# Kernel tuning notes

Hardware: AMD Instinct MI355X
Metric: run time of the kernel (lower is better)

Reference implementation:

```python
import jax, jax.numpy as jnp
import numpy as np

HEAD_SIZE = 64
EMBED_DIM = 1024
SEQ_LEN = 4096
BATCH = 4


def setup_inputs() -> dict:
    key = jax.random.key(0)
    kx, kk, kq, kv = jax.random.split(key, 4)
    x = jax.random.normal(kx, (BATCH, SEQ_LEN, EMBED_DIM), dtype=jnp.float32)
    # nn.Linear(embedding_dim, head_size, bias=False): weight [head_size, embed];
    # store transposed [embed, head_size] so projection is x @ W.
    scale = 1.0 / np.sqrt(EMBED_DIM)
    Wk = jax.random.uniform(kk, (EMBED_DIM, HEAD_SIZE), jnp.float32, -scale, scale)
    Wq = jax.random.uniform(kq, (EMBED_DIM, HEAD_SIZE), jnp.float32, -scale, scale)
    Wv = jax.random.uniform(kv, (EMBED_DIM, HEAD_SIZE), jnp.float32, -scale, scale)
    return {"x": x, "Wk": Wk, "Wq": Wq, "Wv": Wv}


def reference(x, Wk, Wq, Wv):
    B, T, C = x.shape
    k = x @ Wk  # [B, T, H]
    q = x @ Wq  # [B, T, H]
    v = x @ Wv  # [B, T, H]
    H = k.shape[-1]
    s = jnp.einsum('bth,bsh->bts', q, k) * (H ** -0.5)  # [B, T, T]
    causal = jnp.tril(jnp.ones((T, T), dtype=bool))
    s = jnp.where(causal, s, -jnp.inf)
    a = jax.nn.softmax(s, axis=-1)  # dropout p=0.0 -> identity
    z = jnp.einsum('bts,bsh->bth', a, v)  # [B, T, H]
    return z
```

## Files before the change

### kernel.cpp

```cpp
#include <hip/hip_runtime.h>

#define SEQ 4096
#define EMB 1024
#define HS 64

typedef __attribute__((ext_vector_type(8))) short bf16x8;
typedef __attribute__((ext_vector_type(4))) short bf16x4;
typedef __attribute__((ext_vector_type(4))) float f32x4;

__device__ __forceinline__ unsigned short f2b(float f) {
    union { float f; unsigned u; } v; v.f = f;
    unsigned r = v.u + 0x7fffu + ((v.u >> 16) & 1u);
    return (unsigned short)(r >> 16);
}
__device__ __forceinline__ float b2f(unsigned short h) {
    union { unsigned u; float f; } v; v.u = ((unsigned)h) << 16;
    return v.f;
}
__device__ __forceinline__ unsigned cvtpk(float a, float b) {
    unsigned r;
    asm("v_cvt_pk_bf16_f32 %0, %1, %2" : "=v"(r) : "v"(a), "v"(b));
    return r;
}
template <typename T>
__device__ __forceinline__ void gll16(const T* g, void* l) {
    __builtin_amdgcn_global_load_lds(
        (const __attribute__((address_space(1))) unsigned int*)(g),
        (__attribute__((address_space(3))) unsigned int*)(l), 16, 0, 0);
}

__global__ __launch_bounds__(256) void wt_kernel(const float* __restrict__ Wq,
                                                 const float* __restrict__ Wk,
                                                 const float* __restrict__ Wv,
                                                 unsigned short* __restrict__ Wt) {
    int id = blockIdx.x * 256 + threadIdx.x;
    int mat = id >> 16;
    int rem = id & 65535;
    int k = rem >> 6;
    int n = rem & 63;
    const float* W = (mat == 0) ? Wq : (mat == 1) ? Wk : Wv;
    float scale = (mat == 0) ? 0.125f * 1.44269504f : 1.0f;
    Wt[(mat * HS + n) * EMB + k] = f2b(W[k * HS + n] * scale);
}

__global__ __launch_bounds__(256, 2) void proj_kernel(const float* __restrict__ x,
                                                      const unsigned short* __restrict__ Wt,
                                                      unsigned short* __restrict__ Qb,
                                                      unsigned short* __restrict__ Kb,
                                                      unsigned short* __restrict__ Vt) {
    __shared__ float xf[2][32 * 64];
    __shared__ unsigned short wb[2][192 * 64];
    const int tid = threadIdx.x;
    const int wave = tid >> 6, lane = tid & 63;
    const int col = lane & 15, quad = lane >> 4;
    const int m0 = blockIdx.x * 32;
    const int b = m0 >> 12, t0 = m0 & 4095;

    const int xr_in = lane >> 4;
    const int xc = lane & 15;
    const int wr_in = lane >> 3;
    const int wc = lane & 7;

    f32x4 acc[2][3];
    #pragma unroll
    for (int i = 0; i < 2; i++)
        #pragma unroll
        for (int j = 0; j < 3; j++) acc[i][j] = (f32x4){0.f, 0.f, 0.f, 0.f};

    auto stage = [&](int k0, int bufi) {
        #pragma unroll
        for (int t = 0; t < 2; t++) {
            int R = (wave + t * 4) * 4;
            int row = R + xr_in;
            gll16(x + (size_t)(m0 + row) * EMB + k0 + ((xc ^ (row & 15)) << 2),
                  &xf[bufi][R * 64]);
        }
        #pragma unroll
        for (int t = 0; t < 6; t++) {
            int R = (wave * 6 + t) * 8;
            int row = R + wr_in;
            gll16(Wt + (size_t)row * EMB + k0 + ((wc ^ (row & 7)) << 3),
                  &wb[bufi][R * 64]);
        }
    };

    stage(0, 0);
    int buf = 0;
    #pragma unroll 1
    for (int k0 = 0; k0 < EMB; k0 += 64) {
        __syncthreads();
        if (k0 + 64 < EMB) stage(k0 + 64, buf ^ 1);
        #pragma unroll
        for (int kc = 0; kc < 2; kc++) {
            const int q2 = quad + kc * 4;
            bf16x8 af[2], bfr[3];
            #pragma unroll
            for (int mt = 0; mt < 2; mt++) {
                int rr = mt * 16 + col;
                float4 lo = *(const float4*)&xf[buf][rr * 64 + (((2 * q2) ^ col) << 2)];
                float4 hi = *(const float4*)&xf[buf][rr * 64 + (((2 * q2 + 1) ^ col) << 2)];
                bf16x8 a;
                a[0] = (short)f2b(lo.x); a[1] = (short)f2b(lo.y);
                a[2] = (short)f2b(lo.z); a[3] = (short)f2b(lo.w);
                a[4] = (short)f2b(hi.x); a[5] = (short)f2b(hi.y);
                a[6] = (short)f2b(hi.z); a[7] = (short)f2b(hi.w);
                af[mt] = a;
            }
            #pragma unroll
            for (int nt = 0; nt < 3; nt++) {
                int rn = wave * 48 + nt * 16 + col;
                bfr[nt] = *(const bf16x8*)&wb[buf][rn * 64 + ((q2 ^ (col & 7)) << 3)];
            }
            #pragma unroll
            for (int mt = 0; mt < 2; mt++)
                #pragma unroll
                for (int nt = 0; nt < 3; nt++)
                    acc[mt][nt] = __builtin_amdgcn_mfma_f32_16x16x32_bf16(af[mt], bfr[nt], acc[mt][nt], 0, 0, 0);
        }
        buf ^= 1;
    }

    #pragma unroll
    for (int mt = 0; mt < 2; mt++)
        #pragma unroll
        for (int nt = 0; nt < 3; nt++) {
            const int g = wave * 3 + nt;
            const int mat = g >> 2;
            const int ncol = (g & 3) * 16 + col;
            #pragma unroll
            for (int r = 0; r < 4; r++) {
                unsigned short val = f2b(acc[mt][nt][r]);
                int row = mt * 16 + quad * 4 + r;
                if (mat == 0)      Qb[(size_t)(m0 + row) * HS + ncol] = val;
                else if (mat == 1) Kb[(size_t)(m0 + row) * HS + ncol] = val;
                else               Vt[((size_t)b * HS + ncol) * SEQ + t0 + row] = val;
            }
        }
}

__global__ __launch_bounds__(512, 4) void attn_kernel(const unsigned short* __restrict__ Qb,
                                                      const unsigned short* __restrict__ Kb,
                                                      const unsigned short* __restrict__ Vt,
                                                      unsigned short* __restrict__ Opart,
                                                      float* __restrict__ Lpart,
                                                      float* __restrict__ out) {
    __shared__ unsigned short Kl[3][64 * 64];
    __shared__ unsigned short Vl[3][64 * 64];
    const int tid = threadIdx.x;
    const int wave = tid >> 6, lane = tid & 63;
    const int col = lane & 15, quad = lane >> 4;
    const int bid = blockIdx.x;
    const int g = 118 - (bid >> 2);
    const int b = bid & 3;
    int T = 0, accp = 0;
    for (;;) { int np = T / 5 + 1; if (accp + np > g) break; accp += np; T++; }
    const int piece = g - accp;
    const int np = T / 5 + 1;
    const int q0 = T << 7;
    const int s_beg = piece * 10;
    const int s_end = min(s_beg + 10, 2 * T + 2);

    const unsigned short* Kp = Kb + ((size_t)(b << 12)) * HS;
    const unsigned short* Vp = Vt + (size_t)b * HS * SEQ;

    bf16x8 qf[2];
    #pragma unroll
    for (int c = 0; c < 2; c++)
        qf[c] = *(const bf16x8*)(Qb + ((size_t)(b << 12) + q0 + wave * 16 + col) * HS + quad * 8 + c * 32);

    f32x4 o[4];
    float l = 0.f;
    #pragma unroll
    for (int ct = 0; ct < 4; ct++) o[ct] = (f32x4){0.f, 0.f, 0.f, 0.f};

    const int r_in = lane >> 3;
    const int ch = lane & 7;

    auto stage = [&](int s, int bufi) {
        const int kv0 = s << 6;
        int R = wave * 8;
        int row = R + r_in;
        gll16(Kp + (size_t)(kv0 + row) * HS + ((ch ^ (row & 7)) << 3), &Kl[bufi][R * 64]);
        gll16(Vp + (size_t)row * SEQ + kv0 + ((ch ^ (row & 7)) << 3), &Vl[bufi][R * 64]);
    };

    stage(s_beg, 0);
    stage(min(s_beg + 1, s_end - 1), 1);
    int bufr = 0;
    const int grb = (b << 12) + q0 + wave * 16;
    const int qg = q0 + wave * 16 + col;

    #pragma unroll 1
    for (int s = s_beg; s < s_end; s++) {
        asm volatile("s_waitcnt vmcnt(2)\n\ts_barrier" ::: "memory");
        stage(min(s + 2, s_end - 1), (bufr + 2) % 3);
        const int kv0 = s << 6;

        f32x4 sacc[4];
        #pragma unroll
        for (int ct = 0; ct < 4; ct++) sacc[ct] = (f32x4){0.f, 0.f, 0.f, 0.f};
        #pragma unroll
        for (int ct = 0; ct < 4; ct++) {
            int n = ct * 16 + col;
            #pragma unroll
            for (int kc = 0; kc < 2; kc++) {
                bf16x8 kf = *(const bf16x8*)&Kl[bufr][n * 64 + (((kc * 4 + quad) ^ (col & 7)) << 3)];
                sacc[ct] = __builtin_amdgcn_mfma_f32_16x16x32_bf16(kf, qf[kc], sacc[ct], 0, 0, 0);
            }
        }

        float p[4][4];
        #pragma unroll
        for (int ct = 0; ct < 4; ct++) {
            int kvb = kv0 + ct * 16 + quad * 4;
            #pragma unroll
            for (int r = 0; r < 4; r++) {
                float e = __builtin_exp2f(sacc[ct][r]);
                e = (kvb + r > qg) ? 0.f : e;
                p[ct][r] = e;
                l += e;
            }
        }

        bf16x8 pf[2];
        #pragma unroll
        for (int kc = 0; kc < 2; kc++) {
            union { unsigned u[4]; bf16x8 v; } pu;
            pu.u[0] = cvtpk(p[2 * kc][0],     p[2 * kc][1]);
            pu.u[1] = cvtpk(p[2 * kc][2],     p[2 * kc][3]);
            pu.u[2] = cvtpk(p[2 * kc + 1][0], p[2 * kc + 1][1]);
            pu.u[3] = cvtpk(p[2 * kc + 1][2], p[2 * kc + 1][3]);
            pf[kc] = pu.v;
        }

        #pragma unroll
        for (int ct = 0; ct < 4; ct++) {
            const unsigned short* Vrow = &Vl[bufr][(ct * 16 + col) * 64];
            #pragma unroll
            for (int kc = 0; kc < 2; kc++) {
                int c0 = ((kc << 2) + (quad >> 1)) ^ (col & 7);
                int c1 = ((kc << 2) + 2 + (quad >> 1)) ^ (col & 7);
                bf16x4 lo = *(const bf16x4*)&Vrow[(c0 << 3) + ((quad & 1) << 2)];
                bf16x4 hi = *(const bf16x4*)&Vrow[(c1 << 3) + ((quad & 1) << 2)];
                bf16x8 vf = __builtin_shufflevector(lo, hi, 0, 1, 2, 3, 4, 5, 6, 7);
                o[ct] = __builtin_amdgcn_mfma_f32_16x16x32_bf16(pf[kc], vf, o[ct], 0, 0, 0);
            }
        }
        bufr = (bufr == 2) ? 0 : bufr + 1;
    }

    l += __shfl_xor(l, 16, 64);
    l += __shfl_xor(l, 32, 64);

    if (np == 1) {
        float lq[4];
        #pragma unroll
        for (int r = 0; r < 4; r++) lq[r] = __shfl(l, quad * 4 + r, 64);
        #pragma unroll
        for (int ct = 0; ct < 4; ct++)
            #pragma unroll
            for (int r = 0; r < 4; r++)
                out[(size_t)(grb + quad * 4 + r) * HS + ct * 16 + col] = o[ct][r] / lq[r];
    } else {
        const int widx = bid * 8 + wave;
        unsigned short* Op = Opart + (size_t)widx * 1024;
        #pragma unroll
        for (int ct = 0; ct < 4; ct++) {
            ushort4 st;
            st.x = f2b(o[ct][0]); st.y = f2b(o[ct][1]);
            st.z = f2b(o[ct][2]); st.w = f2b(o[ct][3]);
            *(ushort4*)(Op + ct * 256 + lane * 4) = st;
        }
        if (quad == 0) Lpart[widx * 16 + col] = l;
    }
}

__global__ __launch_bounds__(256) void comb_kernel(const unsigned short* __restrict__ Opart,
                                                   const float* __restrict__ Lpart,
                                                   float* __restrict__ out) {
    const int bid = blockIdx.x;
    const int b = bid & 3;
    const int idx = bid >> 2;
    const int T = 5 + (idx % 27);
    const int wave = idx / 27;
    const int tid = threadIdx.x;
    const int lane = tid & 63, ct = tid >> 6;
    const int col = lane & 15, quad = lane >> 4;

    const int q = T / 5, r5 = T % 5;
    const int base = T + 5 * q * (q - 1) / 2 + r5 * q;
    const int np = q + 1;

    float acc[4] = {0.f, 0.f, 0.f, 0.f};
    float l[4] = {0.f, 0.f, 0.f, 0.f};
    for (int p = 0; p < np; p++) {
        int gg = base + p;
        int bidp = ((118 - gg) << 2) | b;
        int widx = bidp * 8 + wave;
        ushort4 v = *(const ushort4*)(Opart + (size_t)widx * 1024 + ct * 256 + lane * 4);
        acc[0] += b2f(v.x); acc[1] += b2f(v.y);
        acc[2] += b2f(v.z); acc[3] += b2f(v.w);
        #pragma unroll
        for (int r = 0; r < 4; r++)
            l[r] += Lpart[widx * 16 + quad * 4 + r];
    }
    const size_t rowb = (size_t)(b << 12) + (T << 7) + wave * 16 + quad * 4;
    #pragma unroll
    for (int r = 0; r < 4; r++)
        out[(rowb + r) * HS + ct * 16 + col] = acc[r] / l[r];
}

extern "C" void kernel_launch(void* const* d_in, const int* in_sizes, int n_in,
                              void* d_out, int out_size, void* d_ws, size_t ws_size,
                              hipStream_t stream) {
    const float* x  = (const float*)d_in[0];
    const float* Wk = (const float*)d_in[1];
    const float* Wq = (const float*)d_in[2];
    const float* Wv = (const float*)d_in[3];
    float* out = (float*)d_out;

    char* ws = (char*)d_ws;
    unsigned short* Wt = (unsigned short*)(ws);
    unsigned short* Qb = (unsigned short*)(ws + 393216);
    unsigned short* Kb = (unsigned short*)(ws + 2490368);
    unsigned short* Vt = (unsigned short*)(ws + 4587520);
    unsigned short* Opart = (unsigned short*)(ws + 6684672);
    float* Lpart          = (float*)(ws + 14483456);

    wt_kernel<<<dim3(768), dim3(256), 0, stream>>>(Wq, Wk, Wv, Wt);
    proj_kernel<<<dim3(512), dim3(256), 0, stream>>>(x, Wt, Qb, Kb, Vt);
    attn_kernel<<<dim3(476), dim3(512), 0, stream>>>(Qb, Kb, Vt, Opart, Lpart, out);
    comb_kernel<<<dim3(864), dim3(256), 0, stream>>>(Opart, Lpart, out);
}
```

Baseline: 146.9 us.

## Give each attention wave two query tiles to reuse K/V LDS fragments

The attention block shrinks from 8 waves to 4, and each wave now computes two 16-row query tiles. Each K and V fragment read from LDS therefore feeds two MFMAs, halving LDS read traffic per unit of compute and raising per-wave ILP. Each wave stages twice as many K/V rows, and the wait count is adjusted to match. The cost is more registers per wave (launch bounds now 256 threads with min 3 blocks) and fewer waves for latency hiding. The Opart/Lpart indexing is kept compatible with the combine kernel.

```diff
diff --git a/kernel.cpp b/kernel.cpp
--- a/kernel.cpp
+++ b/kernel.cpp
@@ -138,7 +138,7 @@
         }
 }
 
-__global__ __launch_bounds__(512, 4) void attn_kernel(const unsigned short* __restrict__ Qb,
+__global__ __launch_bounds__(256, 3) void attn_kernel(const unsigned short* __restrict__ Qb,
                                                       const unsigned short* __restrict__ Kb,
                                                       const unsigned short* __restrict__ Vt,
                                                       unsigned short* __restrict__ Opart,
@@ -163,74 +163,87 @@
     const unsigned short* Kp = Kb + ((size_t)(b << 12)) * HS;
     const unsigned short* Vp = Vt + (size_t)b * HS * SEQ;
 
-    bf16x8 qf[2];
-    #pragma unroll
-    for (int c = 0; c < 2; c++)
-        qf[c] = *(const bf16x8*)(Qb + ((size_t)(b << 12) + q0 + wave * 16 + col) * HS + quad * 8 + c * 32);
-
-    f32x4 o[4];
-    float l = 0.f;
-    #pragma unroll
-    for (int ct = 0; ct < 4; ct++) o[ct] = (f32x4){0.f, 0.f, 0.f, 0.f};
+    bf16x8 qf[2][2];
+    #pragma unroll
+    for (int mq = 0; mq < 2; mq++)
+        #pragma unroll
+        for (int c = 0; c < 2; c++)
+            qf[mq][c] = *(const bf16x8*)(Qb + ((size_t)(b << 12) + q0 + wave * 32 + mq * 16 + col) * HS + quad * 8 + c * 32);
+
+    f32x4 o[2][4];
+    float l[2] = {0.f, 0.f};
+    #pragma unroll
+    for (int mq = 0; mq < 2; mq++)
+        #pragma unroll
+        for (int ct = 0; ct < 4; ct++) o[mq][ct] = (f32x4){0.f, 0.f, 0.f, 0.f};
 
     const int r_in = lane >> 3;
     const int ch = lane & 7;
 
     auto stage = [&](int s, int bufi) {
         const int kv0 = s << 6;
-        int R = wave * 8;
-        int row = R + r_in;
-        gll16(Kp + (size_t)(kv0 + row) * HS + ((ch ^ (row & 7)) << 3), &Kl[bufi][R * 64]);
-        gll16(Vp + (size_t)row * SEQ + kv0 + ((ch ^ (row & 7)) << 3), &Vl[bufi][R * 64]);
+        #pragma unroll
+        for (int t = 0; t < 2; t++) {
+            int R = wave * 16 + t * 8;
+            int row = R + r_in;
+            gll16(Kp + (size_t)(kv0 + row) * HS + ((ch ^ (row & 7)) << 3), &Kl[bufi][R * 64]);
+            gll16(Vp + (size_t)row * SEQ + kv0 + ((ch ^ (row & 7)) << 3), &Vl[bufi][R * 64]);
+        }
     };
 
     stage(s_beg, 0);
     stage(min(s_beg + 1, s_end - 1), 1);
     int bufr = 0;
-    const int grb = (b << 12) + q0 + wave * 16;
-    const int qg = q0 + wave * 16 + col;
+    const int grb = (b << 12) + q0 + wave * 32;
+    const int qgb = q0 + wave * 32 + col;
 
     #pragma unroll 1
     for (int s = s_beg; s < s_end; s++) {
-        asm volatile("s_waitcnt vmcnt(2)\n\ts_barrier" ::: "memory");
+        asm volatile("s_waitcnt vmcnt(4)\n\ts_barrier" ::: "memory");
         stage(min(s + 2, s_end - 1), (bufr + 2) % 3);
         const int kv0 = s << 6;
 
-        f32x4 sacc[4];
-        #pragma unroll
-        for (int ct = 0; ct < 4; ct++) sacc[ct] = (f32x4){0.f, 0.f, 0.f, 0.f};
+        f32x4 sacc[2][4];
+        #pragma unroll
+        for (int mq = 0; mq < 2; mq++)
+            #pragma unroll
+            for (int ct = 0; ct < 4; ct++) sacc[mq][ct] = (f32x4){0.f, 0.f, 0.f, 0.f};
         #pragma unroll
         for (int ct = 0; ct < 4; ct++) {
             int n = ct * 16 + col;
             #pragma unroll
             for (int kc = 0; kc < 2; kc++) {
                 bf16x8 kf = *(const bf16x8*)&Kl[bufr][n * 64 + (((kc * 4 + quad) ^ (col & 7)) << 3)];
-                sacc[ct] = __builtin_amdgcn_mfma_f32_16x16x32_bf16(kf, qf[kc], sacc[ct], 0, 0, 0);
-            }
-        }
-
-        float p[4][4];
-        #pragma unroll
-        for (int ct = 0; ct < 4; ct++) {
-            int kvb = kv0 + ct * 16 + quad * 4;
-            #pragma unroll
-            for (int r = 0; r < 4; r++) {
-                float e = __builtin_exp2f(sacc[ct][r]);
-                e = (kvb + r > qg) ? 0.f : e;
-                p[ct][r] = e;
-                l += e;
-            }
-        }
-
-        bf16x8 pf[2];
-        #pragma unroll
-        for (int kc = 0; kc < 2; kc++) {
-            union { unsigned u[4]; bf16x8 v; } pu;
-            pu.u[0] = cvtpk(p[2 * kc][0],     p[2 * kc][1]);
-            pu.u[1] = cvtpk(p[2 * kc][2],     p[2 * kc][3]);
-            pu.u[2] = cvtpk(p[2 * kc + 1][0], p[2 * kc + 1][1]);
-            pu.u[3] = cvtpk(p[2 * kc + 1][2], p[2 * kc + 1][3]);
-            pf[kc] = pu.v;
+                sacc[0][ct] = __builtin_amdgcn_mfma_f32_16x16x32_bf16(kf, qf[0][kc], sacc[0][ct], 0, 0, 0);
+                sacc[1][ct] = __builtin_amdgcn_mfma_f32_16x16x32_bf16(kf, qf[1][kc], sacc[1][ct], 0, 0, 0);
+            }
+        }
+
+        bf16x8 pf[2][2];
+        #pragma unroll
+        for (int mq = 0; mq < 2; mq++) {
+            const int qg = qgb + mq * 16;
+            float p[4][4];
+            #pragma unroll
+            for (int ct = 0; ct < 4; ct++) {
+                int kvb = kv0 + ct * 16 + quad * 4;
+                #pragma unroll
+                for (int r = 0; r < 4; r++) {
+                    float e = __builtin_exp2f(sacc[mq][ct][r]);
+                    e = (kvb + r > qg) ? 0.f : e;
+                    p[ct][r] = e;
+                    l[mq] += e;
+                }
+            }
+            #pragma unroll
+            for (int kc = 0; kc < 2; kc++) {
+                union { unsigned u[4]; bf16x8 v; } pu;
+                pu.u[0] = cvtpk(p[2 * kc][0],     p[2 * kc][1]);
+                pu.u[1] = cvtpk(p[2 * kc][2],     p[2 * kc][3]);
+                pu.u[2] = cvtpk(p[2 * kc + 1][0], p[2 * kc + 1][1]);
+                pu.u[3] = cvtpk(p[2 * kc + 1][2], p[2 * kc + 1][3]);
+                pf[mq][kc] = pu.v;
+            }
         }
 
         #pragma unroll
@@ -243,35 +256,45 @@
                 bf16x4 lo = *(const bf16x4*)&Vrow[(c0 << 3) + ((quad & 1) << 2)];
                 bf16x4 hi = *(const bf16x4*)&Vrow[(c1 << 3) + ((quad & 1) << 2)];
                 bf16x8 vf = __builtin_shufflevector(lo, hi, 0, 1, 2, 3, 4, 5, 6, 7);
-                o[ct] = __builtin_amdgcn_mfma_f32_16x16x32_bf16(pf[kc], vf, o[ct], 0, 0, 0);
+                o[0][ct] = __builtin_amdgcn_mfma_f32_16x16x32_bf16(pf[0][kc], vf, o[0][ct], 0, 0, 0);
+                o[1][ct] = __builtin_amdgcn_mfma_f32_16x16x32_bf16(pf[1][kc], vf, o[1][ct], 0, 0, 0);
             }
         }
         bufr = (bufr == 2) ? 0 : bufr + 1;
     }
 
-    l += __shfl_xor(l, 16, 64);
-    l += __shfl_xor(l, 32, 64);
+    #pragma unroll
+    for (int mq = 0; mq < 2; mq++) {
+        l[mq] += __shfl_xor(l[mq], 16, 64);
+        l[mq] += __shfl_xor(l[mq], 32, 64);
+    }
 
     if (np == 1) {
-        float lq[4];
-        #pragma unroll
-        for (int r = 0; r < 4; r++) lq[r] = __shfl(l, quad * 4 + r, 64);
-        #pragma unroll
-        for (int ct = 0; ct < 4; ct++)
-            #pragma unroll
-            for (int r = 0; r < 4; r++)
-                out[(size_t)(grb + quad * 4 + r) * HS + ct * 16 + col] = o[ct][r] / lq[r];
+        #pragma unroll
+        for (int mq = 0; mq < 2; mq++) {
+            float lq[4];
+            #pragma unroll
+            for (int r = 0; r < 4; r++) lq[r] = __shfl(l[mq], quad * 4 + r, 64);
+            #pragma unroll
+            for (int ct = 0; ct < 4; ct++)
+                #pragma unroll
+                for (int r = 0; r < 4; r++)
+                    out[(size_t)(grb + mq * 16 + quad * 4 + r) * HS + ct * 16 + col] = o[mq][ct][r] / lq[r];
+        }
     } else {
-        const int widx = bid * 8 + wave;
-        unsigned short* Op = Opart + (size_t)widx * 1024;
-        #pragma unroll
-        for (int ct = 0; ct < 4; ct++) {
-            ushort4 st;
-            st.x = f2b(o[ct][0]); st.y = f2b(o[ct][1]);
-            st.z = f2b(o[ct][2]); st.w = f2b(o[ct][3]);
-            *(ushort4*)(Op + ct * 256 + lane * 4) = st;
-        }
-        if (quad == 0) Lpart[widx * 16 + col] = l;
+        #pragma unroll
+        for (int mq = 0; mq < 2; mq++) {
+            const int widx = bid * 8 + wave * 2 + mq;
+            unsigned short* Op = Opart + (size_t)widx * 1024;
+            #pragma unroll
+            for (int ct = 0; ct < 4; ct++) {
+                ushort4 st;
+                st.x = f2b(o[mq][ct][0]); st.y = f2b(o[mq][ct][1]);
+                st.z = f2b(o[mq][ct][2]); st.w = f2b(o[mq][ct][3]);
+                *(ushort4*)(Op + ct * 256 + lane * 4) = st;
+            }
+            if (quad == 0) Lpart[widx * 16 + col] = l[mq];
+        }
     }
 }
 
@@ -329,6 +352,6 @@
 
     wt_kernel<<<dim3(768), dim3(256), 0, stream>>>(Wq, Wk, Wv, Wt);
     proj_kernel<<<dim3(512), dim3(256), 0, stream>>>(x, Wt, Qb, Kb, Vt);
-    attn_kernel<<<dim3(476), dim3(512), 0, stream>>>(Qb, Kb, Vt, Opart, Lpart, out);
+    attn_kernel<<<dim3(476), dim3(256), 0, stream>>>(Qb, Kb, Vt, Opart, Lpart, out);
     comb_kernel<<<dim3(864), dim3(256), 0, stream>>>(Opart, Lpart, out);
 }
```

After: 146.1 us. About the same (-0.6%).
